# Performance work log

Hardware: AMD Instinct MI355X
Metric: run time of the kernel (lower is better)

Reference implementation:

```python
import jax, jax.numpy as jnp
import numpy as np

N = 50000       # nodes
E = 800000      # edges
D_IN = 128      # input_dim
HID = 256       # hidden_dim
HEADS = 4
FH = HID // 4   # per-head out dim = 64
OUT = 8         # output_dim
NEG_SLOPE = 0.2 # GATConv leaky_relu slope


def setup_inputs() -> dict:
    key = jax.random.key(0)
    ks = jax.random.split(key, 16)
    def glorot(k, shape):
        fan_in, fan_out = shape[0], shape[-1]
        s = jnp.sqrt(6.0 / (fan_in + fan_out))
        return jax.random.uniform(k, shape, jnp.float32, -s, s)
    inp = {
        "x": jax.random.normal(ks[0], (N, D_IN), jnp.float32),
        "edge_index": jax.random.randint(ks[1], (2, E), 0, N, jnp.int64),
        # GCN layers
        "W1": glorot(ks[2], (D_IN, HID)), "b1": jnp.zeros((HID,), jnp.float32),
        "W2": glorot(ks[3], (HID, HID)), "b2": jnp.zeros((HID,), jnp.float32),
        "W3": glorot(ks[4], (HID, HID // 2)), "b3": jnp.zeros((HID // 2,), jnp.float32),
        # GAT layer: in = HID//2 = 128, out per head = FH, 4 heads concat -> HID
        "Wg": glorot(ks[5], (HID // 2, HEADS * FH)),
        "a_src": glorot(ks[6], (HEADS, FH)),
        "a_dst": glorot(ks[7], (HEADS, FH)),
        "bg": jnp.zeros((HEADS * FH,), jnp.float32),
        # classifier MLP: HID -> HID//2 -> HID//4 -> OUT
        "Wc1": glorot(ks[8], (HID, HID // 2)), "bc1": jnp.zeros((HID // 2,), jnp.float32),
        "Wc2": glorot(ks[9], (HID // 2, HID // 4)), "bc2": jnp.zeros((HID // 4,), jnp.float32),
        "Wc3": glorot(ks[10], (HID // 4, OUT)), "bc3": jnp.zeros((OUT,), jnp.float32),
    }
    return inp


def _with_self_loops(edge_index, n):
    loop = jnp.arange(n, dtype=edge_index.dtype)
    src = jnp.concatenate([edge_index[0], loop])
    dst = jnp.concatenate([edge_index[1], loop])
    return src, dst


def gcn_conv(x, W, b, src, dst, n):
    # PyG GCNConv: h = X W; out = D^{-1/2}(A+I)D^{-1/2} h + b (self loops in src/dst)
    h = x @ W
    deg = jax.ops.segment_sum(jnp.ones_like(dst, jnp.float32), dst, num_segments=n)
    dinv = jnp.where(deg > 0, jax.lax.rsqrt(deg), 0.0)
    norm = dinv[src] * dinv[dst]                      # [E+N]
    out = jax.ops.segment_sum(h[src] * norm[:, None], dst, num_segments=n)
    return out + b


def gat_conv(x, Wg, a_src, a_dst, bg, src, dst, n):
    # PyG GATConv (eval mode, no attn dropout), self loops included in src/dst
    h = (x @ Wg).reshape(n, HEADS, FH)                # [N,H,F]
    al_s = jnp.einsum('nhf,hf->nh', h, a_src)         # [N,H]
    al_d = jnp.einsum('nhf,hf->nh', h, a_dst)
    e = jax.nn.leaky_relu(al_s[src] + al_d[dst], NEG_SLOPE)  # [E+N,H]
    m = jax.ops.segment_max(e, dst, num_segments=n)   # per-dst stable softmax
    ex = jnp.exp(e - m[dst])
    den = jax.ops.segment_sum(ex, dst, num_segments=n)
    alpha = ex / den[dst]                             # [E+N,H]
    out = jax.ops.segment_sum(h[src] * alpha[:, :, None], dst, num_segments=n)
    return out.reshape(n, HEADS * FH) + bg


def reference(x, edge_index, W1, b1, W2, b2, W3, b3, Wg, a_src, a_dst, bg,
              Wc1, bc1, Wc2, bc2, Wc3, bc3):
    n = x.shape[0]
    src, dst = _with_self_loops(edge_index, n)
    h1 = jax.nn.relu(gcn_conv(x, W1, b1, src, dst, n))
    h2 = jax.nn.relu(gcn_conv(h1, W2, b2, src, dst, n)) + h1
    h3 = jax.nn.relu(gcn_conv(h2, W3, b3, src, dst, n))
    h_att = jax.nn.relu(gat_conv(h3, Wg, a_src, a_dst, bg, src, dst, n))
    h_pooled = jnp.mean(h_att, axis=0, keepdims=True)           # [1, HID]
    z = jax.nn.relu(h_pooled @ Wc1 + bc1)
    z = jax.nn.relu(z @ Wc2 + bc2)
    return z @ Wc3 + bc3                                        # [1, OUT]
```

## Files before the change

### kernel.cpp

```cpp
#include <hip/hip_runtime.h>
#include <hip/hip_bf16.h>

#define NNODES 50000
#define NEDGES 800000
#define EN 850000
#define SCAN_B 196

typedef __attribute__((ext_vector_type(8))) short bf16x8;
typedef __attribute__((ext_vector_type(4))) float f32x4;

__device__ __forceinline__ float bf2f(unsigned short u) {
    return __uint_as_float(((unsigned)u) << 16);
}
__device__ __forceinline__ float bflo(unsigned u) { return __uint_as_float(u << 16); }
__device__ __forceinline__ float bfhi(unsigned u) { return __uint_as_float(u & 0xffff0000u); }
__device__ __forceinline__ unsigned short f2bf(float x) {
    unsigned u = __float_as_uint(x);
    u += 0x7fffu + ((u >> 16) & 1u);
    return (unsigned short)(u >> 16);
}
__device__ __forceinline__ unsigned pack2bf(float a, float b) {
    return (unsigned)f2bf(a) | ((unsigned)f2bf(b) << 16);
}

__global__ __launch_bounds__(256) void deg_kernel(const int* __restrict__ ei, float* __restrict__ deg) {
    int e = blockIdx.x * blockDim.x + threadIdx.x;
    if (e < NEDGES) atomicAdd(&deg[ei[NEDGES + e]], 1.0f);
}

__global__ __launch_bounds__(256) void dinv_kernel(const float* __restrict__ deg, float* __restrict__ dinv) {
    int i = blockIdx.x * blockDim.x + threadIdx.x;
    if (i < NNODES) dinv[i] = rsqrtf(deg[i] + 1.0f);
}

__global__ __launch_bounds__(256) void scan_part1(const float* __restrict__ deg, int* __restrict__ row,
                                                  int* __restrict__ bsum) {
    __shared__ int sdata[256];
    int t = threadIdx.x;
    int idx = blockIdx.x * 256 + t;
    int v = idx < NNODES ? (int)deg[idx] + 1 : 0;
    sdata[t] = v;
    __syncthreads();
    for (int off = 1; off < 256; off <<= 1) {
        int tmp = t >= off ? sdata[t - off] : 0;
        __syncthreads();
        sdata[t] += tmp;
        __syncthreads();
    }
    if (idx < NNODES) row[idx] = sdata[t] - v;
    if (t == 255) bsum[blockIdx.x] = sdata[255];
}

__global__ __launch_bounds__(256) void scan_part2(int* __restrict__ bsum, int* __restrict__ bofs,
                                                  int* __restrict__ row) {
    __shared__ int sdata[256];
    int t = threadIdx.x;
    int v = t < SCAN_B ? bsum[t] : 0;
    sdata[t] = v;
    __syncthreads();
    for (int off = 1; off < 256; off <<= 1) {
        int tmp = t >= off ? sdata[t - off] : 0;
        __syncthreads();
        sdata[t] += tmp;
        __syncthreads();
    }
    if (t < SCAN_B) bofs[t] = sdata[t] - v;
    if (t == 0) row[NNODES] = EN;
}

__global__ __launch_bounds__(256) void scan_part3(int* __restrict__ row, const int* __restrict__ bofs) {
    int idx = blockIdx.x * 256 + threadIdx.x;
    if (idx < NNODES) row[idx] += bofs[blockIdx.x];
}

__global__ __launch_bounds__(256) void scatter_kernel(const int* __restrict__ ei, const int* __restrict__ row,
                                                      int* __restrict__ cursor, const float* __restrict__ dinv,
                                                      uint2* __restrict__ csr) {
    int e = blockIdx.x * blockDim.x + threadIdx.x;
    if (e >= EN) return;
    int s, d;
    if (e < NEDGES) { s = ei[e]; d = ei[NEDGES + e]; } else { s = e - NEDGES; d = s; }
    int pos = row[d] + atomicAdd(&cursor[d], 1);
    csr[pos] = make_uint2((unsigned)s, __float_as_uint(dinv[s] * dinv[d]));
}

__global__ __launch_bounds__(256) void tobf16_kernel(const float* __restrict__ in, unsigned short* __restrict__ out,
                                                     int total8) {
    int i = blockIdx.x * 256 + threadIdx.x;
    if (i >= total8) return;
    float4 a = *(const float4*)&in[(size_t)i * 8];
    float4 b = *(const float4*)&in[(size_t)i * 8 + 4];
    uint4 o;
    o.x = pack2bf(a.x, a.y); o.y = pack2bf(a.z, a.w);
    o.z = pack2bf(b.x, b.y); o.w = pack2bf(b.z, b.w);
    *(uint4*)&out[(size_t)i * 8] = o;
}

__device__ __forceinline__ void split_bf(float x, unsigned short& h, unsigned short& l) {
    unsigned u = __float_as_uint(x);
    h = (unsigned short)(u >> 16);
    float r = x - __uint_as_float(u & 0xffff0000u);
    l = (unsigned short)(__float_as_uint(r) >> 16);
}

__global__ __launch_bounds__(256) void wsplit_kernel(const float* __restrict__ W, unsigned short* __restrict__ Wh,
                                                     unsigned short* __restrict__ Wl, int K, int N) {
    int idx = blockIdx.x * 256 + threadIdx.x;
    if (idx >= K * N) return;
    int n = idx / K, k = idx % K;
    unsigned short h, l;
    split_bf(W[(size_t)k * N + n], h, l);
    Wh[idx] = h; Wl[idx] = l;
}

template<int MODE>
__global__ __launch_bounds__(256) void gemm_bf(const unsigned short* __restrict__ A,
                                               const unsigned short* __restrict__ Wth,
                                               const unsigned short* __restrict__ Wtl,
                                               const float* __restrict__ bias,
                                               unsigned short* __restrict__ C, int M, int K, int Nc) {
    __shared__ unsigned short As[128][40];
    __shared__ unsigned short Bh[128][40], Bl[128][40];
    int t = threadIdx.x;
    int row0 = blockIdx.x * 128, col0 = blockIdx.y * 128;
    int lane = t & 63, w = t >> 6;
    int mb = (w >> 1) * 64, nb = (w & 1) * 64;
    int lr = lane & 15, kg = (lane >> 4) * 8;

    f32x4 acc[4][4];
#pragma unroll
    for (int i = 0; i < 4; ++i)
#pragma unroll
        for (int j = 0; j < 4; ++j) acc[i][j] = (f32x4){0.f, 0.f, 0.f, 0.f};

    for (int k0 = 0; k0 < K; k0 += 32) {
#pragma unroll
        for (int it = 0; it < 2; ++it) {
            int q = it * 256 + t;
            int row = q >> 2, seg = (q & 3) * 8;
            int grow = row0 + row;
            uint4 v = make_uint4(0, 0, 0, 0);
            if (grow < M) v = *(const uint4*)&A[(size_t)grow * K + k0 + seg];
            *(uint4*)&As[row][seg] = v;
        }
#pragma unroll
        for (int it = 0; it < 2; ++it) {
            int o = it * 256 + t;
            int n = o >> 2, ko = (o & 3) * 8;
            size_t g = (size_t)(col0 + n) * K + k0 + ko;
            *(uint4*)&Bh[n][ko] = *(const uint4*)&Wth[g];
            *(uint4*)&Bl[n][ko] = *(const uint4*)&Wtl[g];
        }
        __syncthreads();

        bf16x8 a[4], bh[4], bl[4];
#pragma unroll
        for (int mf = 0; mf < 4; ++mf) a[mf] = *(const bf16x8*)&As[mb + mf * 16 + lr][kg];
#pragma unroll
        for (int nf = 0; nf < 4; ++nf) {
            bh[nf] = *(const bf16x8*)&Bh[nb + nf * 16 + lr][kg];
            bl[nf] = *(const bf16x8*)&Bl[nb + nf * 16 + lr][kg];
        }
#pragma unroll
        for (int mf = 0; mf < 4; ++mf)
#pragma unroll
            for (int nf = 0; nf < 4; ++nf) {
                acc[mf][nf] = __builtin_amdgcn_mfma_f32_16x16x32_bf16(a[mf], bh[nf], acc[mf][nf], 0, 0, 0);
                acc[mf][nf] = __builtin_amdgcn_mfma_f32_16x16x32_bf16(a[mf], bl[nf], acc[mf][nf], 0, 0, 0);
            }
        __syncthreads();
    }

#pragma unroll
    for (int nf = 0; nf < 4; ++nf) {
        int col = col0 + nb + nf * 16 + lr;
        float bv = (MODE == 1) ? bias[col] : 0.f;
#pragma unroll
        for (int mf = 0; mf < 4; ++mf) {
#pragma unroll
            for (int r = 0; r < 4; ++r) {
                int row = row0 + mb + mf * 16 + (lane >> 4) * 4 + r;
                if (row < M) {
                    float v = acc[mf][nf][r];
                    if (MODE == 1) v = fmaxf(v + bv, 0.f);
                    C[(size_t)row * Nc + col] = f2bf(v);
                }
            }
        }
    }
}

template<int NC, int MODE>
__global__ __launch_bounds__(256) void gcn_agg_bf(const unsigned short* __restrict__ h, const int* __restrict__ row,
                                                  const uint2* __restrict__ csr,
                                                  const float* __restrict__ b, const unsigned short* __restrict__ res,
                                                  unsigned short* __restrict__ out) {
    int wid = (int)((blockIdx.x * blockDim.x + threadIdx.x) >> 6);
    if (wid >= NNODES) return;
    int lane = threadIdx.x & 63;
    constexpr int LPE = NC / 8;
    constexpr int EPI = 64 / LPE;
    int sub = lane / LPE, li = lane % LPE;
    int col = li * 8;
    float acc[8];
#pragma unroll
    for (int i = 0; i < 8; ++i) acc[i] = 0.f;
    int j0 = row[wid], j1 = row[wid + 1];
    for (int j = j0 + sub; j < j1; j += EPI) {
        uint2 sw = csr[j];
        float wg = __uint_as_float(sw.y);
        uint4 v = *(const uint4*)&h[(size_t)sw.x * NC + col];
        acc[0] += bflo(v.x) * wg; acc[1] += bfhi(v.x) * wg;
        acc[2] += bflo(v.y) * wg; acc[3] += bfhi(v.y) * wg;
        acc[4] += bflo(v.z) * wg; acc[5] += bfhi(v.z) * wg;
        acc[6] += bflo(v.w) * wg; acc[7] += bfhi(v.w) * wg;
    }
#pragma unroll
    for (int i = 0; i < 8; ++i) {
        acc[i] += __shfl_xor(acc[i], 32);
        if constexpr (EPI == 4) acc[i] += __shfl_xor(acc[i], 16);
    }
    if (lane < LPE) {
        if constexpr (MODE >= 1) {
#pragma unroll
            for (int i = 0; i < 8; ++i) acc[i] = fmaxf(acc[i] + b[col + i], 0.f);
        }
        if constexpr (MODE == 2) {
            uint4 rv = *(const uint4*)&res[(size_t)wid * NC + col];
            acc[0] += bflo(rv.x); acc[1] += bfhi(rv.x);
            acc[2] += bflo(rv.y); acc[3] += bfhi(rv.y);
            acc[4] += bflo(rv.z); acc[5] += bfhi(rv.z);
            acc[6] += bflo(rv.w); acc[7] += bfhi(rv.w);
        }
        uint4 o;
        o.x = pack2bf(acc[0], acc[1]); o.y = pack2bf(acc[2], acc[3]);
        o.z = pack2bf(acc[4], acc[5]); o.w = pack2bf(acc[6], acc[7]);
        *(uint4*)&out[(size_t)wid * NC + col] = o;
    }
}

__global__ __launch_bounds__(256) void att_logits(const unsigned short* __restrict__ hg,
                                                  const float* __restrict__ a_src, const float* __restrict__ a_dst,
                                                  float* __restrict__ als, float* __restrict__ ald) {
    int gid = blockIdx.x * blockDim.x + threadIdx.x;
    if (gid >= NNODES * 4) return;
    int n = gid >> 2, h = gid & 3;
    const unsigned short* hr = hg + (size_t)n * 256 + h * 64;
    const float* as_ = a_src + h * 64;
    const float* ad_ = a_dst + h * 64;
    float s1 = 0.f, s2 = 0.f;
#pragma unroll
    for (int f = 0; f < 64; f += 8) {
        uint4 v = *(const uint4*)&hr[f];
        float x0 = bflo(v.x), x1 = bfhi(v.x), x2 = bflo(v.y), x3 = bfhi(v.y);
        float x4 = bflo(v.z), x5 = bfhi(v.z), x6 = bflo(v.w), x7 = bfhi(v.w);
        s1 += x0 * as_[f] + x1 * as_[f + 1] + x2 * as_[f + 2] + x3 * as_[f + 3]
            + x4 * as_[f + 4] + x5 * as_[f + 5] + x6 * as_[f + 6] + x7 * as_[f + 7];
        s2 += x0 * ad_[f] + x1 * ad_[f + 1] + x2 * ad_[f + 2] + x3 * ad_[f + 3]
            + x4 * ad_[f + 4] + x5 * ad_[f + 5] + x6 * ad_[f + 6] + x7 * ad_[f + 7];
    }
    als[gid] = s1; ald[gid] = s2;
}

__device__ __forceinline__ float lrelu(float x) { return x < 0.f ? 0.2f * x : x; }

__global__ __launch_bounds__(256) void gat_csr(const unsigned short* __restrict__ hg, const int* __restrict__ row,
                                               const uint2* __restrict__ csr, const float* __restrict__ als,
                                               const float* __restrict__ ald, const float* __restrict__ bg,
                                               unsigned short* __restrict__ out) {
    int wid = (int)((blockIdx.x * blockDim.x + threadIdx.x) >> 6);
    if (wid >= NNODES) return;
    int lane = threadIdx.x & 63;
    int j0 = row[wid], j1 = row[wid + 1];
    float4 ad = *(const float4*)&ald[wid * 4];

    float m0 = -1e30f, m1 = -1e30f, m2 = -1e30f, m3 = -1e30f;
    for (int j = j0 + lane; j < j1; j += 64) {
        int s = (int)csr[j].x;
        float4 as4 = *(const float4*)&als[s * 4];
        m0 = fmaxf(m0, lrelu(as4.x + ad.x));
        m1 = fmaxf(m1, lrelu(as4.y + ad.y));
        m2 = fmaxf(m2, lrelu(as4.z + ad.z));
        m3 = fmaxf(m3, lrelu(as4.w + ad.w));
    }
#pragma unroll
    for (int off = 32; off >= 1; off >>= 1) {
        m0 = fmaxf(m0, __shfl_xor(m0, off));
        m1 = fmaxf(m1, __shfl_xor(m1, off));
        m2 = fmaxf(m2, __shfl_xor(m2, off));
        m3 = fmaxf(m3, __shfl_xor(m3, off));
    }
    float d0 = 0.f, d1 = 0.f, d2 = 0.f, d3 = 0.f;
    for (int j = j0 + lane; j < j1; j += 64) {
        int s = (int)csr[j].x;
        float4 as4 = *(const float4*)&als[s * 4];
        d0 += __expf(lrelu(as4.x + ad.x) - m0);
        d1 += __expf(lrelu(as4.y + ad.y) - m1);
        d2 += __expf(lrelu(as4.z + ad.z) - m2);
        d3 += __expf(lrelu(as4.w + ad.w) - m3);
    }
#pragma unroll
    for (int off = 32; off >= 1; off >>= 1) {
        d0 += __shfl_xor(d0, off);
        d1 += __shfl_xor(d1, off);
        d2 += __shfl_xor(d2, off);
        d3 += __shfl_xor(d3, off);
    }
    int sub = lane >> 5, li = lane & 31;
    int h = li >> 3;
    float mh   = h == 0 ? m0 : h == 1 ? m1 : h == 2 ? m2 : m3;
    float invh = 1.f / (h == 0 ? d0 : h == 1 ? d1 : h == 2 ? d2 : d3);
    float adh  = h == 0 ? ad.x : h == 1 ? ad.y : h == 2 ? ad.z : ad.w;
    int col = li * 8;
    float acc[8];
#pragma unroll
    for (int i = 0; i < 8; ++i) acc[i] = 0.f;
    for (int j = j0 + sub; j < j1; j += 2) {
        int s = (int)csr[j].x;
        float e = lrelu(als[s * 4 + h] + adh);
        float alpha = __expf(e - mh) * invh;
        uint4 v = *(const uint4*)&hg[(size_t)s * 256 + col];
        acc[0] += bflo(v.x) * alpha; acc[1] += bfhi(v.x) * alpha;
        acc[2] += bflo(v.y) * alpha; acc[3] += bfhi(v.y) * alpha;
        acc[4] += bflo(v.z) * alpha; acc[5] += bfhi(v.z) * alpha;
        acc[6] += bflo(v.w) * alpha; acc[7] += bfhi(v.w) * alpha;
    }
#pragma unroll
    for (int i = 0; i < 8; ++i) acc[i] += __shfl_xor(acc[i], 32);
    if (lane < 32) {
        uint4 o;
        o.x = pack2bf(fmaxf(acc[0] + bg[col], 0.f),     fmaxf(acc[1] + bg[col + 1], 0.f));
        o.y = pack2bf(fmaxf(acc[2] + bg[col + 2], 0.f), fmaxf(acc[3] + bg[col + 3], 0.f));
        o.z = pack2bf(fmaxf(acc[4] + bg[col + 4], 0.f), fmaxf(acc[5] + bg[col + 5], 0.f));
        o.w = pack2bf(fmaxf(acc[6] + bg[col + 6], 0.f), fmaxf(acc[7] + bg[col + 7], 0.f));
        *(uint4*)&out[(size_t)wid * 256 + col] = o;
    }
}

__global__ __launch_bounds__(256) void pool_kernel(const unsigned short* __restrict__ hatt, float* __restrict__ pooled) {
    int col = threadIdx.x;
    int r0 = blockIdx.x * 256;
    int r1 = r0 + 256 < NNODES ? r0 + 256 : NNODES;
    float s = 0.f;
    for (int r = r0; r < r1; ++r) s += bf2f(hatt[(size_t)r * 256 + col]);
    atomicAdd(&pooled[col], s);
}

__global__ __launch_bounds__(256) void mlp_kernel(const float* __restrict__ pooled,
                                                  const float* __restrict__ Wc1, const float* __restrict__ bc1,
                                                  const float* __restrict__ Wc2, const float* __restrict__ bc2,
                                                  const float* __restrict__ Wc3, const float* __restrict__ bc3,
                                                  float* __restrict__ out) {
    __shared__ float p[256], z1[128], z2[64];
    int t = threadIdx.x;
    p[t] = pooled[t] * (1.0f / NNODES);
    __syncthreads();
    if (t < 128) {
        float s = bc1[t];
        for (int k = 0; k < 256; ++k) s += p[k] * Wc1[k * 128 + t];
        z1[t] = fmaxf(s, 0.f);
    }
    __syncthreads();
    if (t < 64) {
        float s = bc2[t];
        for (int k = 0; k < 128; ++k) s += z1[k] * Wc2[k * 64 + t];
        z2[t] = fmaxf(s, 0.f);
    }
    __syncthreads();
    if (t < 8) {
        float s = bc3[t];
        for (int k = 0; k < 64; ++k) s += z2[k] * Wc3[k * 8 + t];
        out[t] = s;
    }
}

extern "C" void kernel_launch(void* const* d_in, const int* in_sizes, int n_in,
                              void* d_out, int out_size, void* d_ws, size_t ws_size,
                              hipStream_t stream) {
    const float* x   = (const float*)d_in[0];
    const int*   ei  = (const int*)d_in[1];
    const float* W1  = (const float*)d_in[2];  const float* b1  = (const float*)d_in[3];
    const float* W2  = (const float*)d_in[4];  const float* b2  = (const float*)d_in[5];
    const float* W3  = (const float*)d_in[6];  const float* b3  = (const float*)d_in[7];
    const float* Wg  = (const float*)d_in[8];
    const float* asr = (const float*)d_in[9];  const float* ads = (const float*)d_in[10];
    const float* bg  = (const float*)d_in[11];
    const float* Wc1 = (const float*)d_in[12]; const float* bc1 = (const float*)d_in[13];
    const float* Wc2 = (const float*)d_in[14]; const float* bc2 = (const float*)d_in[15];
    const float* Wc3 = (const float*)d_in[16]; const float* bc3 = (const float*)d_in[17];
    float* out = (float*)d_out;

    char* w = (char*)d_ws;
    float* deg    = (float*)w; w += (size_t)NNODES * 4;
    float* dinv   = (float*)w; w += (size_t)NNODES * 4;
    int*   rowp   = (int*)w;   w += 200016;
    int*   cursor = (int*)w;   w += (size_t)NNODES * 4;
    int*   bsum   = (int*)w;   w += 256 * 4;
    int*   bofs   = (int*)w;   w += 256 * 4;
    uint2* csr    = (uint2*)w; w += (size_t)EN * 8;
    float* als    = (float*)w; w += (size_t)NNODES * 4 * 4;
    float* ald    = (float*)w; w += (size_t)NNODES * 4 * 4;
    float* pooled = (float*)w; w += 256 * 4;
    unsigned short* W1th = (unsigned short*)w; w += 128 * 256 * 2;
    unsigned short* W1tl = (unsigned short*)w; w += 128 * 256 * 2;
    unsigned short* W2th = (unsigned short*)w; w += 256 * 256 * 2;
    unsigned short* W2tl = (unsigned short*)w; w += 256 * 256 * 2;
    unsigned short* W3th = (unsigned short*)w; w += 256 * 128 * 2;
    unsigned short* W3tl = (unsigned short*)w; w += 256 * 128 * 2;
    unsigned short* Wgth = (unsigned short*)w; w += 128 * 256 * 2;
    unsigned short* Wgtl = (unsigned short*)w; w += 128 * 256 * 2;
    unsigned short* U1 = (unsigned short*)w; w += (size_t)NNODES * 256 * 2;
    unsigned short* U2 = (unsigned short*)w; w += (size_t)NNODES * 256 * 2;
    unsigned short* U3 = (unsigned short*)w; w += (size_t)NNODES * 256 * 2;
    unsigned short* U4 = (unsigned short*)w; w += (size_t)NNODES * 256 * 2;

    hipMemsetAsync(deg, 0, (size_t)NNODES * 4, stream);
    hipMemsetAsync(cursor, 0, (size_t)NNODES * 4, stream);
    deg_kernel<<<(NEDGES + 255) / 256, 256, 0, stream>>>(ei, deg);
    dinv_kernel<<<(NNODES + 255) / 256, 256, 0, stream>>>(deg, dinv);
    scan_part1<<<SCAN_B, 256, 0, stream>>>(deg, rowp, bsum);
    scan_part2<<<1, 256, 0, stream>>>(bsum, bofs, rowp);
    scan_part3<<<SCAN_B, 256, 0, stream>>>(rowp, bofs);
    scatter_kernel<<<(EN + 255) / 256, 256, 0, stream>>>(ei, rowp, cursor, dinv, csr);

    wsplit_kernel<<<(128 * 256 + 255) / 256, 256, 0, stream>>>(W1, W1th, W1tl, 128, 256);
    wsplit_kernel<<<(256 * 256 + 255) / 256, 256, 0, stream>>>(W2, W2th, W2tl, 256, 256);
    wsplit_kernel<<<(256 * 128 + 255) / 256, 256, 0, stream>>>(W3, W3th, W3tl, 256, 128);
    wsplit_kernel<<<(128 * 256 + 255) / 256, 256, 0, stream>>>(Wg, Wgth, Wgtl, 128, 256);
    tobf16_kernel<<<(NNODES * 128 / 8 + 255) / 256, 256, 0, stream>>>(x, U1, NNODES * 128 / 8);

    dim3 gA((NNODES + 127) / 128, 2);
    dim3 gB((NNODES + 127) / 128, 1);
    int aggBlocks = (NNODES * 64 + 255) / 256;

    gcn_agg_bf<128, 0><<<aggBlocks, 256, 0, stream>>>(U1, rowp, csr, nullptr, nullptr, U2);
    gemm_bf<1><<<gA, 256, 0, stream>>>(U2, W1th, W1tl, b1, U3, NNODES, 128, 256);

    gemm_bf<0><<<gA, 256, 0, stream>>>(U3, W2th, W2tl, nullptr, U1, NNODES, 256, 256);
    gcn_agg_bf<256, 2><<<aggBlocks, 256, 0, stream>>>(U1, rowp, csr, b2, U3, U2);

    gemm_bf<0><<<gB, 256, 0, stream>>>(U2, W3th, W3tl, nullptr, U4, NNODES, 256, 128);
    gcn_agg_bf<128, 1><<<aggBlocks, 256, 0, stream>>>(U4, rowp, csr, b3, nullptr, U1);

    gemm_bf<0><<<gA, 256, 0, stream>>>(U1, Wgth, Wgtl, nullptr, U2, NNODES, 128, 256);
    att_logits<<<(NNODES * 4 + 255) / 256, 256, 0, stream>>>(U2, asr, ads, als, ald);
    gat_csr<<<aggBlocks, 256, 0, stream>>>(U2, rowp, csr, als, ald, bg, U3);

    hipMemsetAsync(pooled, 0, 256 * 4, stream);
    pool_kernel<<<(NNODES + 255) / 256, 256, 0, stream>>>(U3, pooled);
    mlp_kernel<<<1, 256, 0, stream>>>(pooled, Wc1, bc1, Wc2, bc2, Wc3, bc3, out);
}
```

Baseline: 574.4 us.

## Fuse setup kernels, unroll gather loops, single-pass softmax for low-degree nodes

Folds the dinv computation into the first scan kernel and merges the four weight-split launches into one kernel, cutting launch count. It unrolls the GCN and GAT gather loops by two so two neighbour rows are loaded in flight at once. For nodes with degree at most 64, the GAT softmax computes the logits once per lane instead of reloading them for a separate max pass and sum pass. This adds code paths and some register pressure in exchange for fewer launches and more memory-level parallelism.

```diff
diff --git a/kernel.cpp b/kernel.cpp
--- a/kernel.cpp
+++ b/kernel.cpp
@@ -22,23 +22,26 @@
 __device__ __forceinline__ unsigned pack2bf(float a, float b) {
     return (unsigned)f2bf(a) | ((unsigned)f2bf(b) << 16);
 }
+__device__ __forceinline__ void acc8(float* acc, uint4 v, float wg) {
+    acc[0] += bflo(v.x) * wg; acc[1] += bfhi(v.x) * wg;
+    acc[2] += bflo(v.y) * wg; acc[3] += bfhi(v.y) * wg;
+    acc[4] += bflo(v.z) * wg; acc[5] += bfhi(v.z) * wg;
+    acc[6] += bflo(v.w) * wg; acc[7] += bfhi(v.w) * wg;
+}
 
 __global__ __launch_bounds__(256) void deg_kernel(const int* __restrict__ ei, float* __restrict__ deg) {
     int e = blockIdx.x * blockDim.x + threadIdx.x;
     if (e < NEDGES) atomicAdd(&deg[ei[NEDGES + e]], 1.0f);
 }
 
-__global__ __launch_bounds__(256) void dinv_kernel(const float* __restrict__ deg, float* __restrict__ dinv) {
-    int i = blockIdx.x * blockDim.x + threadIdx.x;
-    if (i < NNODES) dinv[i] = rsqrtf(deg[i] + 1.0f);
-}
-
 __global__ __launch_bounds__(256) void scan_part1(const float* __restrict__ deg, int* __restrict__ row,
-                                                  int* __restrict__ bsum) {
+                                                  int* __restrict__ bsum, float* __restrict__ dinv) {
     __shared__ int sdata[256];
     int t = threadIdx.x;
     int idx = blockIdx.x * 256 + t;
-    int v = idx < NNODES ? (int)deg[idx] + 1 : 0;
+    float dg = idx < NNODES ? deg[idx] : 0.f;
+    if (idx < NNODES) dinv[idx] = rsqrtf(dg + 1.0f);
+    int v = idx < NNODES ? (int)dg + 1 : 0;
     sdata[t] = v;
     __syncthreads();
     for (int off = 1; off < 256; off <<= 1) {
@@ -103,14 +106,25 @@
     l = (unsigned short)(__float_as_uint(r) >> 16);
 }
 
-__global__ __launch_bounds__(256) void wsplit_kernel(const float* __restrict__ W, unsigned short* __restrict__ Wh,
-                                                     unsigned short* __restrict__ Wl, int K, int N) {
-    int idx = blockIdx.x * 256 + threadIdx.x;
-    if (idx >= K * N) return;
-    int n = idx / K, k = idx % K;
+__device__ __forceinline__ void do_split(const float* W, unsigned short* Wh, unsigned short* Wl,
+                                         int i, int K, int N) {
+    int n = i / K, k = i - n * K;
     unsigned short h, l;
     split_bf(W[(size_t)k * N + n], h, l);
-    Wh[idx] = h; Wl[idx] = l;
+    Wh[i] = h; Wl[i] = l;
+}
+
+__global__ __launch_bounds__(256) void wsplit4_kernel(const float* __restrict__ W1, const float* __restrict__ W2,
+                                                      const float* __restrict__ W3, const float* __restrict__ Wg,
+                                                      unsigned short* __restrict__ W1th, unsigned short* __restrict__ W1tl,
+                                                      unsigned short* __restrict__ W2th, unsigned short* __restrict__ W2tl,
+                                                      unsigned short* __restrict__ W3th, unsigned short* __restrict__ W3tl,
+                                                      unsigned short* __restrict__ Wgth, unsigned short* __restrict__ Wgtl) {
+    int idx = blockIdx.x * 256 + threadIdx.x;
+    if (idx < 32768)        do_split(W1, W1th, W1tl, idx, 128, 256);
+    else if (idx < 98304)   do_split(W2, W2th, W2tl, idx - 32768, 256, 256);
+    else if (idx < 131072)  do_split(W3, W3th, W3tl, idx - 98304, 256, 128);
+    else if (idx < 163840)  do_split(Wg, Wgth, Wgtl, idx - 131072, 128, 256);
 }
 
 template<int MODE>
@@ -206,14 +220,18 @@
 #pragma unroll
     for (int i = 0; i < 8; ++i) acc[i] = 0.f;
     int j0 = row[wid], j1 = row[wid + 1];
-    for (int j = j0 + sub; j < j1; j += EPI) {
-        uint2 sw = csr[j];
-        float wg = __uint_as_float(sw.y);
-        uint4 v = *(const uint4*)&h[(size_t)sw.x * NC + col];
-        acc[0] += bflo(v.x) * wg; acc[1] += bfhi(v.x) * wg;
-        acc[2] += bflo(v.y) * wg; acc[3] += bfhi(v.y) * wg;
-        acc[4] += bflo(v.z) * wg; acc[5] += bfhi(v.z) * wg;
-        acc[6] += bflo(v.w) * wg; acc[7] += bfhi(v.w) * wg;
+    int j = j0 + sub;
+    for (; j + EPI < j1; j += 2 * EPI) {
+        uint2 c0 = csr[j], c1 = csr[j + EPI];
+        uint4 v0 = *(const uint4*)&h[(size_t)c0.x * NC + col];
+        uint4 v1 = *(const uint4*)&h[(size_t)c1.x * NC + col];
+        acc8(acc, v0, __uint_as_float(c0.y));
+        acc8(acc, v1, __uint_as_float(c1.y));
+    }
+    if (j < j1) {
+        uint2 c0 = csr[j];
+        uint4 v0 = *(const uint4*)&h[(size_t)c0.x * NC + col];
+        acc8(acc, v0, __uint_as_float(c0.y));
     }
 #pragma unroll
     for (int i = 0; i < 8; ++i) {
@@ -227,10 +245,7 @@
         }
         if constexpr (MODE == 2) {
             uint4 rv = *(const uint4*)&res[(size_t)wid * NC + col];
-            acc[0] += bflo(rv.x); acc[1] += bfhi(rv.x);
-            acc[2] += bflo(rv.y); acc[3] += bfhi(rv.y);
-            acc[4] += bflo(rv.z); acc[5] += bfhi(rv.z);
-            acc[6] += bflo(rv.w); acc[7] += bfhi(rv.w);
+            acc8(acc, rv, 1.0f);
         }
         uint4 o;
         o.x = pack2bf(acc[0], acc[1]); o.y = pack2bf(acc[2], acc[3]);
@@ -272,40 +287,69 @@
     if (wid >= NNODES) return;
     int lane = threadIdx.x & 63;
     int j0 = row[wid], j1 = row[wid + 1];
+    int deg = j1 - j0;
     float4 ad = *(const float4*)&ald[wid * 4];
 
     float m0 = -1e30f, m1 = -1e30f, m2 = -1e30f, m3 = -1e30f;
-    for (int j = j0 + lane; j < j1; j += 64) {
-        int s = (int)csr[j].x;
-        float4 as4 = *(const float4*)&als[s * 4];
-        m0 = fmaxf(m0, lrelu(as4.x + ad.x));
-        m1 = fmaxf(m1, lrelu(as4.y + ad.y));
-        m2 = fmaxf(m2, lrelu(as4.z + ad.z));
-        m3 = fmaxf(m3, lrelu(as4.w + ad.w));
-    }
-#pragma unroll
-    for (int off = 32; off >= 1; off >>= 1) {
-        m0 = fmaxf(m0, __shfl_xor(m0, off));
-        m1 = fmaxf(m1, __shfl_xor(m1, off));
-        m2 = fmaxf(m2, __shfl_xor(m2, off));
-        m3 = fmaxf(m3, __shfl_xor(m3, off));
-    }
     float d0 = 0.f, d1 = 0.f, d2 = 0.f, d3 = 0.f;
-    for (int j = j0 + lane; j < j1; j += 64) {
-        int s = (int)csr[j].x;
-        float4 as4 = *(const float4*)&als[s * 4];
-        d0 += __expf(lrelu(as4.x + ad.x) - m0);
-        d1 += __expf(lrelu(as4.y + ad.y) - m1);
-        d2 += __expf(lrelu(as4.z + ad.z) - m2);
-        d3 += __expf(lrelu(as4.w + ad.w) - m3);
-    }
-#pragma unroll
-    for (int off = 32; off >= 1; off >>= 1) {
-        d0 += __shfl_xor(d0, off);
-        d1 += __shfl_xor(d1, off);
-        d2 += __shfl_xor(d2, off);
-        d3 += __shfl_xor(d3, off);
-    }
+    if (deg <= 64) {
+        float e0 = -1e30f, e1 = -1e30f, e2 = -1e30f, e3 = -1e30f;
+        if (lane < deg) {
+            int s = (int)csr[j0 + lane].x;
+            float4 as4 = *(const float4*)&als[s * 4];
+            e0 = lrelu(as4.x + ad.x); e1 = lrelu(as4.y + ad.y);
+            e2 = lrelu(as4.z + ad.z); e3 = lrelu(as4.w + ad.w);
+        }
+        m0 = e0; m1 = e1; m2 = e2; m3 = e3;
+#pragma unroll
+        for (int off = 32; off >= 1; off >>= 1) {
+            m0 = fmaxf(m0, __shfl_xor(m0, off));
+            m1 = fmaxf(m1, __shfl_xor(m1, off));
+            m2 = fmaxf(m2, __shfl_xor(m2, off));
+            m3 = fmaxf(m3, __shfl_xor(m3, off));
+        }
+        d0 = __expf(e0 - m0); d1 = __expf(e1 - m1);
+        d2 = __expf(e2 - m2); d3 = __expf(e3 - m3);
+#pragma unroll
+        for (int off = 32; off >= 1; off >>= 1) {
+            d0 += __shfl_xor(d0, off);
+            d1 += __shfl_xor(d1, off);
+            d2 += __shfl_xor(d2, off);
+            d3 += __shfl_xor(d3, off);
+        }
+    } else {
+        for (int j = j0 + lane; j < j1; j += 64) {
+            int s = (int)csr[j].x;
+            float4 as4 = *(const float4*)&als[s * 4];
+            m0 = fmaxf(m0, lrelu(as4.x + ad.x));
+            m1 = fmaxf(m1, lrelu(as4.y + ad.y));
+            m2 = fmaxf(m2, lrelu(as4.z + ad.z));
+            m3 = fmaxf(m3, lrelu(as4.w + ad.w));
+        }
+#pragma unroll
+        for (int off = 32; off >= 1; off >>= 1) {
+            m0 = fmaxf(m0, __shfl_xor(m0, off));
+            m1 = fmaxf(m1, __shfl_xor(m1, off));
+            m2 = fmaxf(m2, __shfl_xor(m2, off));
+            m3 = fmaxf(m3, __shfl_xor(m3, off));
+        }
+        for (int j = j0 + lane; j < j1; j += 64) {
+            int s = (int)csr[j].x;
+            float4 as4 = *(const float4*)&als[s * 4];
+            d0 += __expf(lrelu(as4.x + ad.x) - m0);
+            d1 += __expf(lrelu(as4.y + ad.y) - m1);
+            d2 += __expf(lrelu(as4.z + ad.z) - m2);
+            d3 += __expf(lrelu(as4.w + ad.w) - m3);
+        }
+#pragma unroll
+        for (int off = 32; off >= 1; off >>= 1) {
+            d0 += __shfl_xor(d0, off);
+            d1 += __shfl_xor(d1, off);
+            d2 += __shfl_xor(d2, off);
+            d3 += __shfl_xor(d3, off);
+        }
+    }
+
     int sub = lane >> 5, li = lane & 31;
     int h = li >> 3;
     float mh   = h == 0 ? m0 : h == 1 ? m1 : h == 2 ? m2 : m3;
@@ -315,15 +359,21 @@
     float acc[8];
 #pragma unroll
     for (int i = 0; i < 8; ++i) acc[i] = 0.f;
-    for (int j = j0 + sub; j < j1; j += 2) {
-        int s = (int)csr[j].x;
-        float e = lrelu(als[s * 4 + h] + adh);
-        float alpha = __expf(e - mh) * invh;
-        uint4 v = *(const uint4*)&hg[(size_t)s * 256 + col];
-        acc[0] += bflo(v.x) * alpha; acc[1] += bfhi(v.x) * alpha;
-        acc[2] += bflo(v.y) * alpha; acc[3] += bfhi(v.y) * alpha;
-        acc[4] += bflo(v.z) * alpha; acc[5] += bfhi(v.z) * alpha;
-        acc[6] += bflo(v.w) * alpha; acc[7] += bfhi(v.w) * alpha;
+    int j = j0 + sub;
+    for (; j + 2 < j1; j += 4) {
+        uint2 c0 = csr[j], c1 = csr[j + 2];
+        float a0 = __expf(lrelu(als[c0.x * 4 + h] + adh) - mh) * invh;
+        float a1 = __expf(lrelu(als[c1.x * 4 + h] + adh) - mh) * invh;
+        uint4 v0 = *(const uint4*)&hg[(size_t)c0.x * 256 + col];
+        uint4 v1 = *(const uint4*)&hg[(size_t)c1.x * 256 + col];
+        acc8(acc, v0, a0);
+        acc8(acc, v1, a1);
+    }
+    if (j < j1) {
+        uint2 c0 = csr[j];
+        float a0 = __expf(lrelu(als[c0.x * 4 + h] + adh) - mh) * invh;
+        uint4 v0 = *(const uint4*)&hg[(size_t)c0.x * 256 + col];
+        acc8(acc, v0, a0);
     }
 #pragma unroll
     for (int i = 0; i < 8; ++i) acc[i] += __shfl_xor(acc[i], 32);
@@ -417,16 +467,12 @@
     hipMemsetAsync(deg, 0, (size_t)NNODES * 4, stream);
     hipMemsetAsync(cursor, 0, (size_t)NNODES * 4, stream);
     deg_kernel<<<(NEDGES + 255) / 256, 256, 0, stream>>>(ei, deg);
-    dinv_kernel<<<(NNODES + 255) / 256, 256, 0, stream>>>(deg, dinv);
-    scan_part1<<<SCAN_B, 256, 0, stream>>>(deg, rowp, bsum);
+    scan_part1<<<SCAN_B, 256, 0, stream>>>(deg, rowp, bsum, dinv);
     scan_part2<<<1, 256, 0, stream>>>(bsum, bofs, rowp);
     scan_part3<<<SCAN_B, 256, 0, stream>>>(rowp, bofs);
     scatter_kernel<<<(EN + 255) / 256, 256, 0, stream>>>(ei, rowp, cursor, dinv, csr);
 
-    wsplit_kernel<<<(128 * 256 + 255) / 256, 256, 0, stream>>>(W1, W1th, W1tl, 128, 256);
-    wsplit_kernel<<<(256 * 256 + 255) / 256, 256, 0, stream>>>(W2, W2th, W2tl, 256, 256);
-    wsplit_kernel<<<(256 * 128 + 255) / 256, 256, 0, stream>>>(W3, W3th, W3tl, 256, 128);
-    wsplit_kernel<<<(128 * 256 + 255) / 256, 256, 0, stream>>>(Wg, Wgth, Wgtl, 128, 256);
+    wsplit4_kernel<<<640, 256, 0, stream>>>(W1, W2, W3, Wg, W1th, W1tl, W2th, W2tl, W3th, W3tl, Wgth, Wgtl);
     tobf16_kernel<<<(NNODES * 128 / 8 + 255) / 256, 256, 0, stream>>>(x, U1, NNODES * 128 / 8);
 
     dim3 gA((NNODES + 127) / 128, 2);
```

After: 550.0 us. 1.04x faster.
